# Optimization experiments

Measured on AMD Instinct MI355X. Metric: run time of the kernel, lower is better.

The kernel has to match this reference:

```python
import jax, jax.numpy as jnp
import numpy as np

N_NODES = 50000
N_RAND_EDGES = 500000
N_EDGES = N_RAND_EDGES + N_NODES  # random edges + self loops
IN_CH = 128
HID = 128
OUT_CH = 64
N_LAYERS = 3
N_GRAPHS = 64
NEG_SLOPE = 0.2


def setup_inputs() -> dict:
    key = jax.random.key(0)
    ks = jax.random.split(key, 10)
    x = jax.random.randint(ks[0], (N_NODES,), 0, IN_CH)
    rand_edges = jax.random.randint(ks[1], (2, N_RAND_EDGES), 0, N_NODES)
    self_loops = jnp.tile(jnp.arange(N_NODES)[None, :], (2, 1))
    edge_index = jnp.concatenate([rand_edges, self_loops], axis=1)  # [2, N_EDGES]
    batch = jnp.sort(jax.random.randint(ks[2], (N_NODES,), 0, N_GRAPHS))

    emb = jax.random.normal(ks[3], (IN_CH, IN_CH), dtype=jnp.float32) * 0.05
    # all layers are 128 -> 128 (layer0: in=128, last layer out=hidden=128)
    Ws = jax.random.normal(ks[4], (N_LAYERS, HID, HID), dtype=jnp.float32) * 0.05
    a_src = jax.random.normal(ks[5], (N_LAYERS, HID), dtype=jnp.float32) * 0.05
    a_dst = jax.random.normal(ks[6], (N_LAYERS, HID), dtype=jnp.float32) * 0.05
    bs = jnp.zeros((N_LAYERS, HID), dtype=jnp.float32)
    Wout = jax.random.normal(ks[7], (HID, OUT_CH), dtype=jnp.float32) * 0.05
    bout = jnp.zeros((OUT_CH,), dtype=jnp.float32)
    return {"x": x, "edge_index": edge_index, "batch": batch,
            "emb": emb, "Ws": Ws, "a_src": a_src, "a_dst": a_dst,
            "bs": bs, "Wout": Wout, "bout": bout}


def _gat_conv(h, src, dst, W, asrc, adst, b):
    # h: [N, F_in]; edge j->i means src=j (source), dst=i (target)
    h = h @ W  # [N, F]
    s_src = h @ asrc  # [N]
    s_dst = h @ adst  # [N]
    e = jax.nn.leaky_relu(s_src[src] + s_dst[dst], NEG_SLOPE)  # [E]
    # softmax over incoming edges of each destination node
    m = jax.ops.segment_max(e, dst, num_segments=N_NODES)
    ee = jnp.exp(e - m[dst])
    denom = jax.ops.segment_sum(ee, dst, num_segments=N_NODES)
    coef = ee / denom[dst]  # [E]
    out = jax.ops.segment_sum(coef[:, None] * h[src], dst, num_segments=N_NODES)
    return out + b


def reference(x, edge_index, batch, emb, Ws, a_src, a_dst, bs, Wout, bout):
    src, dst = edge_index[0], edge_index[1]
    h = emb[x]  # [N, IN_CH]
    for l in range(N_LAYERS):
        h = _gat_conv(h, src, dst, Ws[l], a_src[l], a_dst[l], bs[l])
        if l < N_LAYERS - 1:
            h = jax.nn.relu(h)
    # global mean pool over graphs
    sums = jax.ops.segment_sum(h, batch, num_segments=N_GRAPHS)
    cnts = jax.ops.segment_sum(jnp.ones((N_NODES,), h.dtype), batch, num_segments=N_GRAPHS)
    pooled = sums / jnp.maximum(cnts, 1.0)[:, None]  # [G, HID]
    return pooled @ Wout + bout  # [G, OUT_CH]
```

## Files before the change

### kernel.cpp

```cpp
#include <hip/hip_runtime.h>

#define NN 50000
#define NE 550000
#define NRE 500000
#define CH 128
#define NG 64
#define OC 64

typedef _Float16 f16x8 __attribute__((ext_vector_type(8)));
typedef float f32x4 __attribute__((ext_vector_type(4)));

#define SCAT_BLOCKS ((NRE + 255) / 256)
#define PREP_BLOCKS ((3 * CH * CH) / 256)

__global__ __launch_bounds__(256) void k_build(const int* __restrict__ src,
                                               const int* __restrict__ dst,
                                               int* __restrict__ cnt,
                                               unsigned short* __restrict__ csr,
                                               const float* __restrict__ Ws,
                                               _Float16* __restrict__ Wt) {
  int b = blockIdx.x;
  if (b < SCAT_BLOCKS) {
    int e = b * 256 + threadIdx.x;
    if (e < NRE) {
      int d = dst[e];
      int pos = atomicAdd(&cnt[d], 1);
      if (pos < 64) csr[(d << 6) + pos] = (unsigned short)src[e];
    }
  } else {
    int idx = (b - SCAT_BLOCKS) * 256 + threadIdx.x;
    int l = idx >> 14, rem = idx & 16383;
    int n = rem >> 7, k = rem & 127;
    Wt[idx] = (_Float16)Ws[(l << 14) + (k << 7) + n];
  }
}

__global__ __launch_bounds__(256) void k_gemm(const float* __restrict__ Xf,
                                              const int* __restrict__ xmap,
                                              const _Float16* __restrict__ Xh,
                                              const _Float16* __restrict__ Wt,
                                              const float* __restrict__ asrc,
                                              const float* __restrict__ adst,
                                              _Float16* __restrict__ hwb,
                                              float* __restrict__ ssrc,
                                              float* __restrict__ sdst) {
  __shared__ _Float16 Al[64][136];
  __shared__ _Float16 Bl[128][136];
  int tid = threadIdx.x;
  int block0 = blockIdx.x * 64;

  if (Xh) {
#pragma unroll
    for (int jj = 0; jj < 4; ++jj) {
      int o = tid + jj * 256;
      int r = o >> 4, k0 = (o & 15) << 3;
      int gr = block0 + r;
      f16x8 h;
#pragma unroll
      for (int q = 0; q < 8; ++q) h[q] = (_Float16)0.f;
      if (gr < NN) h = *(const f16x8*)&Xh[(size_t)gr * CH + k0];
      *(f16x8*)&Al[r][k0] = h;
    }
  } else {
#pragma unroll
    for (int jj = 0; jj < 4; ++jj) {
      int o = tid + jj * 256;
      int r = o >> 4, k0 = (o & 15) << 3;
      int gr = block0 + r;
      float4 v0 = make_float4(0.f, 0.f, 0.f, 0.f);
      float4 v1 = make_float4(0.f, 0.f, 0.f, 0.f);
      if (gr < NN) {
        size_t row = xmap ? (size_t)xmap[gr] : (size_t)gr;
        v0 = *(const float4*)&Xf[row * CH + k0];
        v1 = *(const float4*)&Xf[row * CH + k0 + 4];
      }
      f16x8 h;
      h[0] = (_Float16)v0.x; h[1] = (_Float16)v0.y;
      h[2] = (_Float16)v0.z; h[3] = (_Float16)v0.w;
      h[4] = (_Float16)v1.x; h[5] = (_Float16)v1.y;
      h[6] = (_Float16)v1.z; h[7] = (_Float16)v1.w;
      *(f16x8*)&Al[r][k0] = h;
    }
  }
#pragma unroll
  for (int jj = 0; jj < 8; ++jj) {
    int o = tid + jj * 256;
    int n = o >> 4, k0 = (o & 15) << 3;
    *(f16x8*)&Bl[n][k0] = *(const f16x8*)&Wt[(n << 7) + k0];
  }
  __syncthreads();

  int lane = tid & 63, wave = tid >> 6;
  int quad = lane >> 4, col = lane & 15;
  int row0 = wave << 4;

  f16x8 a[4];
#pragma unroll
  for (int s = 0; s < 4; ++s)
    a[s] = *(const f16x8*)&Al[row0 + col][(s << 5) + (quad << 3)];

  f32x4 acc[8];
#pragma unroll
  for (int t = 0; t < 8; ++t) acc[t] = (f32x4){0.f, 0.f, 0.f, 0.f};

#pragma unroll
  for (int t = 0; t < 8; ++t) {
#pragma unroll
    for (int s = 0; s < 4; ++s) {
      f16x8 b = *(const f16x8*)&Bl[(t << 4) + col][(s << 5) + (quad << 3)];
      acc[t] = __builtin_amdgcn_mfma_f32_16x16x32_f16(a[s], b, acc[t], 0, 0, 0);
    }
  }

  float as_[8], ad_[8];
#pragma unroll
  for (int t = 0; t < 8; ++t) {
    as_[t] = asrc[(t << 4) + col];
    ad_[t] = adst[(t << 4) + col];
  }
#pragma unroll
  for (int r = 0; r < 4; ++r) {
    float ps = 0.f, pd = 0.f;
#pragma unroll
    for (int t = 0; t < 8; ++t) { ps += acc[t][r] * as_[t]; pd += acc[t][r] * ad_[t]; }
#pragma unroll
    for (int o = 1; o < 16; o <<= 1) { ps += __shfl_xor(ps, o); pd += __shfl_xor(pd, o); }
    int gr = block0 + row0 + (quad << 2) + r;
    if (col == 0 && gr < NN) { ssrc[gr] = ps; sdst[gr] = pd; }
  }

  __syncthreads();
#pragma unroll
  for (int t = 0; t < 8; ++t)
#pragma unroll
    for (int r = 0; r < 4; ++r)
      Al[row0 + (quad << 2) + r][(t << 4) + col] = (_Float16)acc[t][r];
  __syncthreads();
#pragma unroll
  for (int jj = 0; jj < 4; ++jj) {
    int o = tid + jj * 256;
    int r = o >> 4, k0 = (o & 15) << 3;
    int gr = block0 + r;
    if (gr < NN) *(f16x8*)&hwb[(size_t)gr * CH + k0] = *(const f16x8*)&Al[r][k0];
  }
}

__global__ __launch_bounds__(256) void k_aggr(const _Float16* __restrict__ hwb,
                                              const float* __restrict__ ssrc,
                                              const float* __restrict__ sdst,
                                              const int* __restrict__ cnt,
                                              const unsigned short* __restrict__ csr,
                                              const float* __restrict__ bias,
                                              float* __restrict__ outf,
                                              _Float16* __restrict__ outh,
                                              int relu) {
  int node = blockIdx.x * 4 + (threadIdx.x >> 6);
  int lane = threadIdx.x & 63;
  if (node >= NN) return;
  int degR = cnt[node];
  degR = degR < 63 ? degR : 63;
  int deg = degR + 1;
  float sd = sdst[node];

  int s = (lane < degR) ? (int)csr[(node << 6) + lane] : node;
  float srcsc = ssrc[s];

  int cl = lane & 15, eg = lane >> 4;
  int c = cl << 3;

  f16x8 zro;
#pragma unroll
  for (int q = 0; q < 8; ++q) zro[q] = (_Float16)0.f;

  int p0 = __shfl(s, eg);
  int p1 = __shfl(s, eg + 4);
  int p2 = __shfl(s, eg + 8);
  int p3 = __shfl(s, eg + 12);
  f16x8 r0 = zro, r1 = zro, r2 = zro, r3 = zro;
  if (eg < deg)      r0 = *(const f16x8*)&hwb[(size_t)p0 * CH + c];
  if (eg + 4 < deg)  r1 = *(const f16x8*)&hwb[(size_t)p1 * CH + c];
  if (eg + 8 < deg)  r2 = *(const f16x8*)&hwb[(size_t)p2 * CH + c];
  if (eg + 12 < deg) r3 = *(const f16x8*)&hwb[(size_t)p3 * CH + c];

  float e = srcsc + sd;
  e = (e > 0.f) ? e : 0.2f * e;
  float ev = (lane < deg) ? e : -3.0e38f;
#pragma unroll
  for (int o = 32; o; o >>= 1) ev = fmaxf(ev, __shfl_xor(ev, o));
  float ex = (lane < deg) ? __expf(e - ev) : 0.f;
  float ssum = ex;
#pragma unroll
  for (int o = 32; o; o >>= 1) ssum += __shfl_xor(ssum, o);
  float w = ex * __frcp_rn(ssum);

  float a[8] = {0.f, 0.f, 0.f, 0.f, 0.f, 0.f, 0.f, 0.f};

  {
    float w0 = __shfl(w, eg);
    float w1 = __shfl(w, eg + 4);
    float w2 = __shfl(w, eg + 8);
    float w3 = __shfl(w, eg + 12);
#pragma unroll
    for (int q = 0; q < 8; ++q) a[q] += w0 * (float)r0[q];
#pragma unroll
    for (int q = 0; q < 8; ++q) a[q] += w1 * (float)r1[q];
#pragma unroll
    for (int q = 0; q < 8; ++q) a[q] += w2 * (float)r2[q];
#pragma unroll
    for (int q = 0; q < 8; ++q) a[q] += w3 * (float)r3[q];
  }

  int nit = (deg + 15) >> 4;
  for (int jj = 1; jj < nit; ++jj) {
    int ib = (jj << 4) + eg;
    int s0 = __shfl(s, ib);
    int s1 = __shfl(s, ib + 4);
    int s2 = __shfl(s, ib + 8);
    int s3 = __shfl(s, ib + 12);
    float w0 = __shfl(w, ib);
    float w1 = __shfl(w, ib + 4);
    float w2 = __shfl(w, ib + 8);
    float w3 = __shfl(w, ib + 12);
    f16x8 q0 = zro, q1 = zro, q2 = zro, q3 = zro;
    if (ib < deg)      q0 = *(const f16x8*)&hwb[(size_t)s0 * CH + c];
    if (ib + 4 < deg)  q1 = *(const f16x8*)&hwb[(size_t)s1 * CH + c];
    if (ib + 8 < deg)  q2 = *(const f16x8*)&hwb[(size_t)s2 * CH + c];
    if (ib + 12 < deg) q3 = *(const f16x8*)&hwb[(size_t)s3 * CH + c];
#pragma unroll
    for (int q = 0; q < 8; ++q) a[q] += w0 * (float)q0[q];
#pragma unroll
    for (int q = 0; q < 8; ++q) a[q] += w1 * (float)q1[q];
#pragma unroll
    for (int q = 0; q < 8; ++q) a[q] += w2 * (float)q2[q];
#pragma unroll
    for (int q = 0; q < 8; ++q) a[q] += w3 * (float)q3[q];
  }
#pragma unroll
  for (int o = 16; o <= 32; o <<= 1) {
#pragma unroll
    for (int q = 0; q < 8; ++q) a[q] += __shfl_xor(a[q], o);
  }
  if (eg == 0) {
    float4 b0 = *(const float4*)&bias[c];
    float4 b1 = *(const float4*)&bias[c + 4];
    a[0] += b0.x; a[1] += b0.y; a[2] += b0.z; a[3] += b0.w;
    a[4] += b1.x; a[5] += b1.y; a[6] += b1.z; a[7] += b1.w;
    if (relu) {
#pragma unroll
      for (int q = 0; q < 8; ++q) a[q] = fmaxf(a[q], 0.f);
    }
    if (outh) {
      f16x8 v;
#pragma unroll
      for (int q = 0; q < 8; ++q) v[q] = (_Float16)a[q];
      *(f16x8*)&outh[(size_t)node * CH + c] = v;
    } else {
      float4* o4 = (float4*)&outf[(size_t)node * CH + c];
      o4[0] = make_float4(a[0], a[1], a[2], a[3]);
      o4[1] = make_float4(a[4], a[5], a[6], a[7]);
    }
  }
}

#define POOL_NPB 128
__global__ __launch_bounds__(256) void k_pool(const float* __restrict__ h,
                                              const int* __restrict__ batch,
                                              float* __restrict__ pooled,
                                              float* __restrict__ cnt) {
  int wave = threadIdx.x >> 6;
  int lane = threadIdx.x & 63;
  int c = lane << 1;
  int start = blockIdx.x * POOL_NPB + wave;
  int end = blockIdx.x * POOL_NPB + POOL_NPB;
  if (end > NN) end = NN;

  float ax = 0.f, ay = 0.f;
  int run = 0, cur = -1;
  for (int n = start; n < end; n += 4) {
    int g = batch[n];
    if (g != cur) {
      if (run) {
        atomicAdd(&pooled[cur * CH + c], ax);
        atomicAdd(&pooled[cur * CH + c + 1], ay);
        if (lane == 0) atomicAdd(&cnt[cur], (float)run);
      }
      ax = 0.f; ay = 0.f; run = 0; cur = g;
    }
    float2 hv = *(const float2*)&h[(size_t)n * CH + c];
    ax += hv.x; ay += hv.y; run++;
  }
  if (run) {
    atomicAdd(&pooled[cur * CH + c], ax);
    atomicAdd(&pooled[cur * CH + c + 1], ay);
    if (lane == 0) atomicAdd(&cnt[cur], (float)run);
  }
}

__global__ __launch_bounds__(64) void k_out(const float* __restrict__ pooled,
                                            const float* __restrict__ cnt,
                                            const float* __restrict__ Wout,
                                            const float* __restrict__ bout,
                                            float* __restrict__ out) {
  int g = blockIdx.x, c = threadIdx.x;
  float inv = 1.f / fmaxf(cnt[g], 1.f);
  float acc = 0.f;
  for (int k = 0; k < CH; ++k) acc += pooled[g * CH + k] * Wout[k * OC + c];
  out[g * OC + c] = acc * inv + bout[c];
}

extern "C" void kernel_launch(void* const* d_in, const int* in_sizes, int n_in,
                              void* d_out, int out_size, void* d_ws, size_t ws_size,
                              hipStream_t stream) {
  const int* x = (const int*)d_in[0];
  const int* ei = (const int*)d_in[1];
  const int* batch = (const int*)d_in[2];
  const float* emb = (const float*)d_in[3];
  const float* Ws = (const float*)d_in[4];
  const float* a_src = (const float*)d_in[5];
  const float* a_dst = (const float*)d_in[6];
  const float* bs = (const float*)d_in[7];
  const float* Wout = (const float*)d_in[8];
  const float* bout = (const float*)d_in[9];
  float* out = (float*)d_out;
  const int* esrc = ei;
  const int* edst = ei + NE;

  char* p = (char*)d_ws;
  auto take = [&](size_t n) { char* q = p; p += (n + 255) & ~(size_t)255; return q; };
  float* X = (float*)take((size_t)NN * CH * 4);
  _Float16* Xh = (_Float16*)take((size_t)NN * CH * 2);
  _Float16* Yb = (_Float16*)take((size_t)NN * CH * 2);
  _Float16* Wt = (_Float16*)take((size_t)3 * CH * CH * 2);
  float* ssrc = (float*)take((size_t)NN * 4);
  float* sdst = (float*)take((size_t)NN * 4);
  unsigned short* csr = (unsigned short*)take((size_t)NN * 64 * 2);
  int* cnt = (int*)take((size_t)NN * 4);
  float* pooled = (float*)take((size_t)(NG * CH + NG) * 4);
  float* gcnt = pooled + NG * CH;
  size_t zbytes = (size_t)((char*)p - (char*)cnt);

  hipMemsetAsync(cnt, 0, zbytes, stream);

  k_build<<<SCAT_BLOCKS + PREP_BLOCKS, 256, 0, stream>>>(esrc, edst, cnt, csr,
                                                         Ws, Wt);

  for (int l = 0; l < 3; ++l) {
    k_gemm<<<(NN + 63) / 64, 256, 0, stream>>>(l == 0 ? emb : nullptr,
                                               l == 0 ? x : nullptr,
                                               l == 0 ? nullptr : Xh,
                                               Wt + l * CH * CH,
                                               a_src + l * CH, a_dst + l * CH,
                                               Yb, ssrc, sdst);
    k_aggr<<<(NN + 3) / 4, 256, 0, stream>>>(Yb, ssrc, sdst, cnt, csr,
                                             bs + l * CH,
                                             l < 2 ? nullptr : X,
                                             l < 2 ? Xh : nullptr,
                                             l < 2 ? 1 : 0);
  }
  k_pool<<<(NN + POOL_NPB - 1) / POOL_NPB, 256, 0, stream>>>(X, batch, pooled,
                                                             gcnt);
  k_out<<<NG, OC, 0, stream>>>(pooled, gcnt, Wout, bout, out);
}
```

Before: 259.9 us.

## Fuse mean-pool into last aggregation via per-node atomics, derive counts by binary search

The final GAT aggregation no longer writes fp32 node features; each node atomically adds its output row into the per-graph pooled sums. The separate pooling kernel is removed, and graph counts are computed in the output kernel by binary search on the sorted batch array. This avoids writing and re-reading a large intermediate and one launch, at the cost of many contended float atomics on a small pooled buffer.

```diff
diff --git a/kernel.cpp b/kernel.cpp
--- a/kernel.cpp
+++ b/kernel.cpp
@@ -151,9 +151,9 @@
                                               const int* __restrict__ cnt,
                                               const unsigned short* __restrict__ csr,
                                               const float* __restrict__ bias,
-                                              float* __restrict__ outf,
                                               _Float16* __restrict__ outh,
-                                              int relu) {
+                                              float* __restrict__ pooled,
+                                              const int* __restrict__ batch) {
   int node = blockIdx.x * 4 + (threadIdx.x >> 6);
   int lane = threadIdx.x & 63;
   if (node >= NN) return;
@@ -245,64 +245,34 @@
     float4 b1 = *(const float4*)&bias[c + 4];
     a[0] += b0.x; a[1] += b0.y; a[2] += b0.z; a[3] += b0.w;
     a[4] += b1.x; a[5] += b1.y; a[6] += b1.z; a[7] += b1.w;
-    if (relu) {
+    if (outh) {
 #pragma unroll
       for (int q = 0; q < 8; ++q) a[q] = fmaxf(a[q], 0.f);
-    }
-    if (outh) {
       f16x8 v;
 #pragma unroll
       for (int q = 0; q < 8; ++q) v[q] = (_Float16)a[q];
       *(f16x8*)&outh[(size_t)node * CH + c] = v;
     } else {
-      float4* o4 = (float4*)&outf[(size_t)node * CH + c];
-      o4[0] = make_float4(a[0], a[1], a[2], a[3]);
-      o4[1] = make_float4(a[4], a[5], a[6], a[7]);
-    }
-  }
-}
-
-#define POOL_NPB 128
-__global__ __launch_bounds__(256) void k_pool(const float* __restrict__ h,
-                                              const int* __restrict__ batch,
-                                              float* __restrict__ pooled,
-                                              float* __restrict__ cnt) {
-  int wave = threadIdx.x >> 6;
-  int lane = threadIdx.x & 63;
-  int c = lane << 1;
-  int start = blockIdx.x * POOL_NPB + wave;
-  int end = blockIdx.x * POOL_NPB + POOL_NPB;
-  if (end > NN) end = NN;
-
-  float ax = 0.f, ay = 0.f;
-  int run = 0, cur = -1;
-  for (int n = start; n < end; n += 4) {
-    int g = batch[n];
-    if (g != cur) {
-      if (run) {
-        atomicAdd(&pooled[cur * CH + c], ax);
-        atomicAdd(&pooled[cur * CH + c + 1], ay);
-        if (lane == 0) atomicAdd(&cnt[cur], (float)run);
-      }
-      ax = 0.f; ay = 0.f; run = 0; cur = g;
-    }
-    float2 hv = *(const float2*)&h[(size_t)n * CH + c];
-    ax += hv.x; ay += hv.y; run++;
-  }
-  if (run) {
-    atomicAdd(&pooled[cur * CH + c], ax);
-    atomicAdd(&pooled[cur * CH + c + 1], ay);
-    if (lane == 0) atomicAdd(&cnt[cur], (float)run);
+      int g = batch[node];
+      float* pg = &pooled[g * CH + c];
+#pragma unroll
+      for (int q = 0; q < 8; ++q) atomicAdd(&pg[q], a[q]);
+    }
   }
 }
 
 __global__ __launch_bounds__(64) void k_out(const float* __restrict__ pooled,
-                                            const float* __restrict__ cnt,
+                                            const int* __restrict__ batch,
                                             const float* __restrict__ Wout,
                                             const float* __restrict__ bout,
                                             float* __restrict__ out) {
   int g = blockIdx.x, c = threadIdx.x;
-  float inv = 1.f / fmaxf(cnt[g], 1.f);
+  int lo = 0, hi = NN;
+  while (lo < hi) { int m = (lo + hi) >> 1; if (batch[m] < g) lo = m + 1; else hi = m; }
+  int l2 = lo, h2 = NN;
+  while (l2 < h2) { int m = (l2 + h2) >> 1; if (batch[m] <= g) l2 = m + 1; else h2 = m; }
+  float cntg = (float)(l2 - lo);
+  float inv = 1.f / fmaxf(cntg, 1.f);
   float acc = 0.f;
   for (int k = 0; k < CH; ++k) acc += pooled[g * CH + k] * Wout[k * OC + c];
   out[g * OC + c] = acc * inv + bout[c];
@@ -327,7 +297,6 @@
 
   char* p = (char*)d_ws;
   auto take = [&](size_t n) { char* q = p; p += (n + 255) & ~(size_t)255; return q; };
-  float* X = (float*)take((size_t)NN * CH * 4);
   _Float16* Xh = (_Float16*)take((size_t)NN * CH * 2);
   _Float16* Yb = (_Float16*)take((size_t)NN * CH * 2);
   _Float16* Wt = (_Float16*)take((size_t)3 * CH * CH * 2);
@@ -335,8 +304,7 @@
   float* sdst = (float*)take((size_t)NN * 4);
   unsigned short* csr = (unsigned short*)take((size_t)NN * 64 * 2);
   int* cnt = (int*)take((size_t)NN * 4);
-  float* pooled = (float*)take((size_t)(NG * CH + NG) * 4);
-  float* gcnt = pooled + NG * CH;
+  float* pooled = (float*)take((size_t)NG * CH * 4);
   size_t zbytes = (size_t)((char*)p - (char*)cnt);
 
   hipMemsetAsync(cnt, 0, zbytes, stream);
@@ -353,11 +321,9 @@
                                                Yb, ssrc, sdst);
     k_aggr<<<(NN + 3) / 4, 256, 0, stream>>>(Yb, ssrc, sdst, cnt, csr,
                                              bs + l * CH,
-                                             l < 2 ? nullptr : X,
                                              l < 2 ? Xh : nullptr,
-                                             l < 2 ? 1 : 0);
-  }
-  k_pool<<<(NN + POOL_NPB - 1) / POOL_NPB, 256, 0, stream>>>(X, batch, pooled,
-                                                             gcnt);
-  k_out<<<NG, OC, 0, stream>>>(pooled, gcnt, Wout, bout, out);
-}
+                                             l < 2 ? nullptr : pooled,
+                                             l < 2 ? nullptr : batch);
+  }
+  k_out<<<NG, OC, 0, stream>>>(pooled, batch, Wout, bout, out);
+}
```

Result: slower. 751.5 us (+189.2%).

## Fuse graph build with layer-0 GEMM and fold output projection into pool

Applied to the files above, without the earlier changes.

Merges the CSR scatter and weight transpose into one launch with the first-layer embedding-gather GEMM, which transposes its own layer-0 weights straight from global memory. Removes the separate k_out launch: the last pool block to finish, chosen by an atomic counter, does the mean and output projection, taking group counts from a binary search over the sorted batch array. The aim is fewer kernel launches and less serialization between them. The cost is a strided uncached weight read in every GEMM tile, larger shared memory in the pool kernel, and a serial tail on the last block.

```diff
diff --git a/kernel.cpp b/kernel.cpp
--- a/kernel.cpp
+++ b/kernel.cpp
@@ -6,38 +6,134 @@
 #define CH 128
 #define NG 64
 #define OC 64
+#define POOL_NPB 128
+#define NTILE ((NN + 63) / 64)
+#define NPOOLB ((NN + POOL_NPB - 1) / POOL_NPB)
 
 typedef _Float16 f16x8 __attribute__((ext_vector_type(8)));
 typedef float f32x4 __attribute__((ext_vector_type(4)));
 
 #define SCAT_BLOCKS ((NRE + 255) / 256)
-#define PREP_BLOCKS ((3 * CH * CH) / 256)
-
-__global__ __launch_bounds__(256) void k_build(const int* __restrict__ src,
-                                               const int* __restrict__ dst,
-                                               int* __restrict__ cnt,
-                                               unsigned short* __restrict__ csr,
-                                               const float* __restrict__ Ws,
-                                               _Float16* __restrict__ Wt) {
+#define PREP2_BLOCKS ((2 * CH * CH) / 256)
+
+__global__ __launch_bounds__(256) void k_fused0(
+    const int* __restrict__ x, const int* __restrict__ esrc,
+    const int* __restrict__ edst, const float* __restrict__ emb,
+    const float* __restrict__ Ws, const float* __restrict__ asrc,
+    const float* __restrict__ adst, int* __restrict__ cnt,
+    unsigned short* __restrict__ csr, _Float16* __restrict__ Wt,
+    _Float16* __restrict__ hwb, float* __restrict__ ssrc,
+    float* __restrict__ sdst) {
+  __shared__ _Float16 Al[64][136];
+  __shared__ _Float16 Bl[128][136];
   int b = blockIdx.x;
-  if (b < SCAT_BLOCKS) {
-    int e = b * 256 + threadIdx.x;
-    if (e < NRE) {
-      int d = dst[e];
-      int pos = atomicAdd(&cnt[d], 1);
-      if (pos < 64) csr[(d << 6) + pos] = (unsigned short)src[e];
-    }
-  } else {
-    int idx = (b - SCAT_BLOCKS) * 256 + threadIdx.x;
-    int l = idx >> 14, rem = idx & 16383;
-    int n = rem >> 7, k = rem & 127;
-    Wt[idx] = (_Float16)Ws[(l << 14) + (k << 7) + n];
+  int tid = threadIdx.x;
+
+  if (b >= NTILE) {
+    int eb = b - NTILE;
+    if (eb < SCAT_BLOCKS) {
+      int e = eb * 256 + tid;
+      if (e < NRE) {
+        int d = edst[e];
+        int pos = atomicAdd(&cnt[d], 1);
+        if (pos < 64) csr[(d << 6) + pos] = (unsigned short)esrc[e];
+      }
+    } else {
+      int idx = (eb - SCAT_BLOCKS) * 256 + tid;
+      int l = 1 + (idx >> 14), rem = idx & 16383;
+      int n = rem >> 7, k = rem & 127;
+      Wt[(l << 14) + rem] = (_Float16)Ws[(l << 14) + (k << 7) + n];
+    }
+    return;
+  }
+
+  int block0 = b * 64;
+#pragma unroll
+  for (int jj = 0; jj < 4; ++jj) {
+    int o = tid + jj * 256;
+    int r = o >> 4, k0 = (o & 15) << 3;
+    int gr = block0 + r;
+    float4 v0 = make_float4(0.f, 0.f, 0.f, 0.f);
+    float4 v1 = make_float4(0.f, 0.f, 0.f, 0.f);
+    if (gr < NN) {
+      size_t row = (size_t)x[gr];
+      v0 = *(const float4*)&emb[row * CH + k0];
+      v1 = *(const float4*)&emb[row * CH + k0 + 4];
+    }
+    f16x8 h;
+    h[0] = (_Float16)v0.x; h[1] = (_Float16)v0.y;
+    h[2] = (_Float16)v0.z; h[3] = (_Float16)v0.w;
+    h[4] = (_Float16)v1.x; h[5] = (_Float16)v1.y;
+    h[6] = (_Float16)v1.z; h[7] = (_Float16)v1.w;
+    *(f16x8*)&Al[r][k0] = h;
+  }
+#pragma unroll
+  for (int jj = 0; jj < 8; ++jj) {
+    int o = tid + jj * 256;
+    int n = o >> 4, k0 = (o & 15) << 3;
+    f16x8 h;
+#pragma unroll
+    for (int q = 0; q < 8; ++q) h[q] = (_Float16)Ws[((k0 + q) << 7) + n];
+    *(f16x8*)&Bl[n][k0] = h;
+  }
+  __syncthreads();
+
+  int lane = tid & 63, wave = tid >> 6;
+  int quad = lane >> 4, col = lane & 15;
+  int row0 = wave << 4;
+
+  f16x8 a[4];
+#pragma unroll
+  for (int s = 0; s < 4; ++s)
+    a[s] = *(const f16x8*)&Al[row0 + col][(s << 5) + (quad << 3)];
+
+  f32x4 acc[8];
+#pragma unroll
+  for (int t = 0; t < 8; ++t) acc[t] = (f32x4){0.f, 0.f, 0.f, 0.f};
+
+#pragma unroll
+  for (int t = 0; t < 8; ++t) {
+#pragma unroll
+    for (int s = 0; s < 4; ++s) {
+      f16x8 bb = *(const f16x8*)&Bl[(t << 4) + col][(s << 5) + (quad << 3)];
+      acc[t] = __builtin_amdgcn_mfma_f32_16x16x32_f16(a[s], bb, acc[t], 0, 0, 0);
+    }
+  }
+
+  float as_[8], ad_[8];
+#pragma unroll
+  for (int t = 0; t < 8; ++t) {
+    as_[t] = asrc[(t << 4) + col];
+    ad_[t] = adst[(t << 4) + col];
+  }
+#pragma unroll
+  for (int r = 0; r < 4; ++r) {
+    float ps = 0.f, pd = 0.f;
+#pragma unroll
+    for (int t = 0; t < 8; ++t) { ps += acc[t][r] * as_[t]; pd += acc[t][r] * ad_[t]; }
+#pragma unroll
+    for (int o = 1; o < 16; o <<= 1) { ps += __shfl_xor(ps, o); pd += __shfl_xor(pd, o); }
+    int gr = block0 + row0 + (quad << 2) + r;
+    if (col == 0 && gr < NN) { ssrc[gr] = ps; sdst[gr] = pd; }
+  }
+
+  __syncthreads();
+#pragma unroll
+  for (int t = 0; t < 8; ++t)
+#pragma unroll
+    for (int r = 0; r < 4; ++r)
+      Al[row0 + (quad << 2) + r][(t << 4) + col] = (_Float16)acc[t][r];
+  __syncthreads();
+#pragma unroll
+  for (int jj = 0; jj < 4; ++jj) {
+    int o = tid + jj * 256;
+    int r = o >> 4, k0 = (o & 15) << 3;
+    int gr = block0 + r;
+    if (gr < NN) *(f16x8*)&hwb[(size_t)gr * CH + k0] = *(const f16x8*)&Al[r][k0];
   }
 }
 
-__global__ __launch_bounds__(256) void k_gemm(const float* __restrict__ Xf,
-                                              const int* __restrict__ xmap,
-                                              const _Float16* __restrict__ Xh,
+__global__ __launch_bounds__(256) void k_gemm(const _Float16* __restrict__ Xh,
                                               const _Float16* __restrict__ Wt,
                                               const float* __restrict__ asrc,
                                               const float* __restrict__ adst,
@@ -49,38 +145,16 @@
   int tid = threadIdx.x;
   int block0 = blockIdx.x * 64;
 
-  if (Xh) {
-#pragma unroll
-    for (int jj = 0; jj < 4; ++jj) {
-      int o = tid + jj * 256;
-      int r = o >> 4, k0 = (o & 15) << 3;
-      int gr = block0 + r;
-      f16x8 h;
-#pragma unroll
-      for (int q = 0; q < 8; ++q) h[q] = (_Float16)0.f;
-      if (gr < NN) h = *(const f16x8*)&Xh[(size_t)gr * CH + k0];
-      *(f16x8*)&Al[r][k0] = h;
-    }
-  } else {
-#pragma unroll
-    for (int jj = 0; jj < 4; ++jj) {
-      int o = tid + jj * 256;
-      int r = o >> 4, k0 = (o & 15) << 3;
-      int gr = block0 + r;
-      float4 v0 = make_float4(0.f, 0.f, 0.f, 0.f);
-      float4 v1 = make_float4(0.f, 0.f, 0.f, 0.f);
-      if (gr < NN) {
-        size_t row = xmap ? (size_t)xmap[gr] : (size_t)gr;
-        v0 = *(const float4*)&Xf[row * CH + k0];
-        v1 = *(const float4*)&Xf[row * CH + k0 + 4];
-      }
-      f16x8 h;
-      h[0] = (_Float16)v0.x; h[1] = (_Float16)v0.y;
-      h[2] = (_Float16)v0.z; h[3] = (_Float16)v0.w;
-      h[4] = (_Float16)v1.x; h[5] = (_Float16)v1.y;
-      h[6] = (_Float16)v1.z; h[7] = (_Float16)v1.w;
-      *(f16x8*)&Al[r][k0] = h;
-    }
+#pragma unroll
+  for (int jj = 0; jj < 4; ++jj) {
+    int o = tid + jj * 256;
+    int r = o >> 4, k0 = (o & 15) << 3;
+    int gr = block0 + r;
+    f16x8 h;
+#pragma unroll
+    for (int q = 0; q < 8; ++q) h[q] = (_Float16)0.f;
+    if (gr < NN) h = *(const f16x8*)&Xh[(size_t)gr * CH + k0];
+    *(f16x8*)&Al[r][k0] = h;
   }
 #pragma unroll
   for (int jj = 0; jj < 8; ++jj) {
@@ -262,11 +336,17 @@
   }
 }
 
-#define POOL_NPB 128
 __global__ __launch_bounds__(256) void k_pool(const float* __restrict__ h,
                                               const int* __restrict__ batch,
                                               float* __restrict__ pooled,
-                                              float* __restrict__ cnt) {
+                                              int* __restrict__ done,
+                                              const float* __restrict__ Wout,
+                                              const float* __restrict__ bout,
+                                              float* __restrict__ out) {
+  __shared__ float Pl[NG * CH];
+  __shared__ float Wl[CH * OC];
+  __shared__ float invc[NG];
+  __shared__ int islast;
   int wave = threadIdx.x >> 6;
   int lane = threadIdx.x & 63;
   int c = lane << 1;
@@ -282,7 +362,6 @@
       if (run) {
         atomicAdd(&pooled[cur * CH + c], ax);
         atomicAdd(&pooled[cur * CH + c + 1], ay);
-        if (lane == 0) atomicAdd(&cnt[cur], (float)run);
       }
       ax = 0.f; ay = 0.f; run = 0; cur = g;
     }
@@ -292,20 +371,36 @@
   if (run) {
     atomicAdd(&pooled[cur * CH + c], ax);
     atomicAdd(&pooled[cur * CH + c + 1], ay);
-    if (lane == 0) atomicAdd(&cnt[cur], (float)run);
-  }
-}
-
-__global__ __launch_bounds__(64) void k_out(const float* __restrict__ pooled,
-                                            const float* __restrict__ cnt,
-                                            const float* __restrict__ Wout,
-                                            const float* __restrict__ bout,
-                                            float* __restrict__ out) {
-  int g = blockIdx.x, c = threadIdx.x;
-  float inv = 1.f / fmaxf(cnt[g], 1.f);
-  float acc = 0.f;
-  for (int k = 0; k < CH; ++k) acc += pooled[g * CH + k] * Wout[k * OC + c];
-  out[g * OC + c] = acc * inv + bout[c];
+  }
+
+  __threadfence();
+  __syncthreads();
+  if (threadIdx.x == 0) {
+    int t = atomicAdd(done, 1);
+    islast = (t == NPOOLB - 1);
+  }
+  __syncthreads();
+  if (!islast) return;
+
+  for (int i = threadIdx.x; i < NG * CH; i += 256)
+    Pl[i] = atomicAdd(&pooled[i], 0.0f);
+  for (int i = threadIdx.x; i < CH * OC; i += 256)
+    Wl[i] = Wout[i];
+  if (threadIdx.x < NG) {
+    int g = threadIdx.x;
+    int lo = 0, hi = NN;
+    while (lo < hi) { int m = (lo + hi) >> 1; if (batch[m] < g) lo = m + 1; else hi = m; }
+    int l2 = lo, h2 = NN;
+    while (l2 < h2) { int m = (l2 + h2) >> 1; if (batch[m] <= g) l2 = m + 1; else h2 = m; }
+    invc[g] = 1.f / fmaxf((float)(l2 - lo), 1.f);
+  }
+  __syncthreads();
+  for (int i = threadIdx.x; i < NG * OC; i += 256) {
+    int g = i >> 6, cc = i & 63;
+    float acc = 0.f;
+    for (int k = 0; k < CH; ++k) acc += Pl[g * CH + k] * Wl[k * OC + cc];
+    out[g * OC + cc] = acc * invc[g] + bout[cc];
+  }
 }
 
 extern "C" void kernel_launch(void* const* d_in, const int* in_sizes, int n_in,
@@ -335,29 +430,25 @@
   float* sdst = (float*)take((size_t)NN * 4);
   unsigned short* csr = (unsigned short*)take((size_t)NN * 64 * 2);
   int* cnt = (int*)take((size_t)NN * 4);
-  float* pooled = (float*)take((size_t)(NG * CH + NG) * 4);
-  float* gcnt = pooled + NG * CH;
+  float* pooled = (float*)take((size_t)NG * CH * 4);
+  int* done = (int*)take(4);
   size_t zbytes = (size_t)((char*)p - (char*)cnt);
 
   hipMemsetAsync(cnt, 0, zbytes, stream);
 
-  k_build<<<SCAT_BLOCKS + PREP_BLOCKS, 256, 0, stream>>>(esrc, edst, cnt, csr,
-                                                         Ws, Wt);
-
-  for (int l = 0; l < 3; ++l) {
-    k_gemm<<<(NN + 63) / 64, 256, 0, stream>>>(l == 0 ? emb : nullptr,
-                                               l == 0 ? x : nullptr,
-                                               l == 0 ? nullptr : Xh,
-                                               Wt + l * CH * CH,
-                                               a_src + l * CH, a_dst + l * CH,
-                                               Yb, ssrc, sdst);
+  k_fused0<<<NTILE + SCAT_BLOCKS + PREP2_BLOCKS, 256, 0, stream>>>(
+      x, esrc, edst, emb, Ws, a_src, a_dst, cnt, csr, Wt, Yb, ssrc, sdst);
+
+  k_aggr<<<(NN + 3) / 4, 256, 0, stream>>>(Yb, ssrc, sdst, cnt, csr, bs,
+                                           nullptr, Xh, 1);
+  for (int l = 1; l < 3; ++l) {
+    k_gemm<<<NTILE, 256, 0, stream>>>(Xh, Wt + l * CH * CH, a_src + l * CH,
+                                      a_dst + l * CH, Yb, ssrc, sdst);
     k_aggr<<<(NN + 3) / 4, 256, 0, stream>>>(Yb, ssrc, sdst, cnt, csr,
                                              bs + l * CH,
                                              l < 2 ? nullptr : X,
                                              l < 2 ? Xh : nullptr,
                                              l < 2 ? 1 : 0);
   }
-  k_pool<<<(NN + POOL_NPB - 1) / POOL_NPB, 256, 0, stream>>>(X, batch, pooled,
-                                                             gcnt);
-  k_out<<<NG, OC, 0, stream>>>(pooled, gcnt, Wout, bout, out);
+  k_pool<<<NPOOLB, 256, 0, stream>>>(X, batch, pooled, done, Wout, bout, out);
 }
```

New measurement: 334.8 us. 1.29x slower.
